# Performance work log

Hardware: AMD Instinct MI355X
Metric: run time of the kernel (lower is better)

Reference implementation:

```python
import jax, jax.numpy as jnp
import numpy as np

B, T, C, H = 4, 4096, 1024, 64

def setup_inputs() -> dict:
    key = jax.random.key(0)
    kx, kq, kk, kv = jax.random.split(key, 4)
    x = jax.random.normal(kx, (B, T, C), dtype=jnp.float32)
    Wq = jax.random.normal(kq, (C, H), dtype=jnp.float32) * (C ** -0.5)
    Wk = jax.random.normal(kk, (C, H), dtype=jnp.float32) * (C ** -0.5)
    Wv = jax.random.normal(kv, (C, H), dtype=jnp.float32) * (C ** -0.5)
    return {"x": x, "Wq": Wq, "Wk": Wk, "Wv": Wv}

def reference(x, Wq, Wk, Wv):
    # single-head causal attention, dropout p=0 (eval)
    q = jnp.einsum('btc,ch->bth', x, Wq)  # [B,T,H]
    k = jnp.einsum('btc,ch->bth', x, Wk)
    v = jnp.einsum('btc,ch->bth', x, Wv)
    scale = k.shape[-1] ** -0.5
    scores = jnp.einsum('bth,bsh->bts', q, k) * scale  # [B,T,T]
    causal = jnp.tril(jnp.ones((q.shape[1], q.shape[1]), dtype=bool))
    scores = jnp.where(causal, scores, -jnp.inf)
    weights = jax.nn.softmax(scores, axis=-1)
    out = jnp.einsum('bts,bsh->bth', weights, v)  # [B,T,H]
    return out
```

## Files before the change

kernel.cpp:

```cpp
#include <hip/hip_runtime.h>


typedef short  s16x8 __attribute__((ext_vector_type(8)));
typedef float  f32x4 __attribute__((ext_vector_type(4)));
typedef unsigned u32x2 __attribute__((ext_vector_type(2)));

constexpr int B = 4, T = 4096, C = 1024, H = 64;
constexpr int M = B * T;
constexpr float LOG2E = 1.44269504088896340736f;
constexpr float QSCALE = 0.125f * LOG2E;
constexpr float MBASE  = 4.0f * LOG2E;

__device__ __forceinline__ unsigned short f2bf(float f) {
    union { float f; unsigned u; } v; v.f = f;
    unsigned r = v.u + 0x7fffu + ((v.u >> 16) & 1u);
    return (unsigned short)(r >> 16);
}

__device__ __forceinline__ unsigned cvt_pk_bf16(float lo, float hi) {
    unsigned r;
    asm("v_cvt_pk_bf16_f32 %0, %1, %2" : "=v"(r) : "v"(lo), "v"(hi));
    return r;
}

__device__ __forceinline__ float vexp2(float x) {
    float r;
    asm("v_exp_f32 %0, %1" : "=v"(r) : "v"(x));
    return r;
}

__device__ __forceinline__ void gl_lds16(const void* g, void* l) {
    __builtin_amdgcn_global_load_lds(
        (const __attribute__((address_space(1))) unsigned*)g,
        (__attribute__((address_space(3))) unsigned*)l, 16, 0, 0);
}

__global__ void prep_w(const float* __restrict__ Wq, const float* __restrict__ Wk,
                       const float* __restrict__ Wv, unsigned short* __restrict__ Wt) {
    const int n = blockIdx.x;
    const float* W = (n < 64) ? Wq : (n < 128 ? Wk : Wv);
    const int col = n & 63;
    for (int k = threadIdx.x; k < C; k += blockDim.x)
        Wt[(size_t)n * C + k] = f2bf(W[(size_t)k * H + col]);
}

__global__ __launch_bounds__(512) void qkv_proj(
    const float* __restrict__ x, const unsigned short* __restrict__ Wt,
    unsigned short* __restrict__ Q, unsigned short* __restrict__ K,
    unsigned short* __restrict__ VT) {
    __shared__ __align__(16) unsigned short ldsA[2][32 * 64];
    __shared__ __align__(16) unsigned short ldsB[2][192 * 64];

    const int t = threadIdx.x, lane = t & 63, w = t >> 6;
    const int i = lane & 15, g = lane >> 4;
    const int rowbase = blockIdx.x * 32;
    const int rw = w & 1, nw = w >> 1;

    const int arow = t >> 3, aslot = t & 7;
    const float* aga = x + (size_t)(rowbase + arow) * C + ((aslot ^ (arow & 7)) * 8);
    const int awoff = arow * 64 + aslot * 8;
    const bool astage = (t < 256);

    const int brow8 = lane >> 3, bslot = lane & 7;
    const unsigned short* bga[3];
    int bn0[3];
#pragma unroll
    for (int j = 0; j < 3; ++j) {
        bn0[j] = w * 24 + j * 8;
        bga[j] = Wt + (size_t)(bn0[j] + brow8) * C + ((bslot ^ brow8) * 8);
    }

    f32x4 acc[3];
#pragma unroll
    for (int n = 0; n < 3; ++n) acc[n] = (f32x4){0.f, 0.f, 0.f, 0.f};

    {
#pragma unroll
        for (int j = 0; j < 3; ++j)
            gl_lds16(bga[j], &ldsB[0][bn0[j] * 64]);
        if (astage) {
            f32x4 a0 = *(const f32x4*)(aga);
            f32x4 a1 = *(const f32x4*)(aga + 4);
            union { unsigned u[4]; s16x8 v; } av;
            av.u[0] = cvt_pk_bf16(a0[0], a0[1]);
            av.u[1] = cvt_pk_bf16(a0[2], a0[3]);
            av.u[2] = cvt_pk_bf16(a1[0], a1[1]);
            av.u[3] = cvt_pk_bf16(a1[2], a1[3]);
            *(s16x8*)&ldsA[0][awoff] = av.v;
        }
    }
    __syncthreads();

    for (int it = 0; it < 16; ++it) {
        const int cur = it & 1, nxt = cur ^ 1;
        const int kc = (it + 1) * 64;
        f32x4 a0, a1;
        const bool more = (it < 15);
        if (more) {
            if (astage) {
                a0 = *(const f32x4*)(aga + kc);
                a1 = *(const f32x4*)(aga + kc + 4);
            }
#pragma unroll
            for (int j = 0; j < 3; ++j)
                gl_lds16(bga[j] + kc, &ldsB[nxt][bn0[j] * 64]);
        }
#pragma unroll
        for (int kst = 0; kst < 2; ++kst) {
            const int c = kst * 4 + g;
            s16x8 a = *(const s16x8*)&ldsA[cur][(rw * 16 + i) * 64 + ((c ^ (i & 7)) * 8)];
#pragma unroll
            for (int nt = 0; nt < 3; ++nt) {
                int n = nw * 48 + nt * 16 + i;
                s16x8 b = *(const s16x8*)&ldsB[cur][n * 64 + ((c ^ (i & 7)) * 8)];
                acc[nt] = __builtin_amdgcn_mfma_f32_16x16x32_bf16(a, b, acc[nt], 0, 0, 0);
            }
        }
        if (more && astage) {
            union { unsigned u[4]; s16x8 v; } av;
            av.u[0] = cvt_pk_bf16(a0[0], a0[1]);
            av.u[1] = cvt_pk_bf16(a0[2], a0[3]);
            av.u[2] = cvt_pk_bf16(a1[0], a1[1]);
            av.u[3] = cvt_pk_bf16(a1[2], a1[3]);
            *(s16x8*)&ldsA[nxt][awoff] = av.v;
        }
        __syncthreads();
    }

#pragma unroll
    for (int nt = 0; nt < 3; ++nt) {
        const int base = nw * 48 + nt * 16;
        const int n = base + i;
        if (base >= 128) {
            const int h = n - 128;
            const int bb = rowbase >> 12, tb = rowbase & 4095;
            u32x2 pk;
            pk[0] = cvt_pk_bf16(acc[nt][0], acc[nt][1]);
            pk[1] = cvt_pk_bf16(acc[nt][2], acc[nt][3]);
            *(u32x2*)(VT + (size_t)(bb * H + h) * T + tb + g * 8 + rw * 4) = pk;
        } else if (base >= 64) {
#pragma unroll
            for (int r = 0; r < 4; ++r)
                K[(size_t)(rowbase + rw * 16 + g * 4 + r) * H + (n - 64)] = f2bf(acc[nt][r]);
        } else {
#pragma unroll
            for (int r = 0; r < 4; ++r)
                Q[(size_t)(rowbase + rw * 16 + g * 4 + r) * H + n] = f2bf(acc[nt][r] * QSCALE);
        }
    }
}

template<int CUR>
__device__ __forceinline__ void attn_tile(
    int n, int nTiles, int sp, int q0w, int i, int g, int g4, int w,
    int r8, int sl, int sx,
    const unsigned short* Kb, const unsigned short* Vb,
    unsigned short (&ks)[3][64 * 64], unsigned short (&vs)[3][64 * 64],
    const s16x8& bqa0, const s16x8& bqa1, const s16x8& bqb0, const s16x8& bqb1,
    const s16x8& ones, const f32x4& minit,
    f32x4 (&oa)[4], f32x4 (&ob)[4], f32x4& al, f32x4& bl) {
    constexpr int NXT = (CUR + 2) % 3;
    const int kv = (sp + n * 8) * 64;
    const bool issue = (n + 2 < nTiles);

    if (issue) {
        const int kvn = kv + 1024;
#pragma unroll
        for (int j = 0; j < 2; ++j) {
            const int row = (w + j * 4) * 8 + r8;
            gl_lds16(Kb + (size_t)(kvn + row) * H + sx * 8, &ks[NXT][row * 64 + sl * 8]);
            gl_lds16(Vb + (size_t)row * T + kvn + sx * 8,   &vs[NXT][row * 64 + sl * 8]);
        }
    }

    if (kv <= q0w + 31) {
        s16x8 kb[8];
#pragma unroll
        for (int kst = 0; kst < 2; ++kst)
#pragma unroll
            for (int nt = 0; nt < 4; ++nt)
                kb[kst * 4 + nt] = *(const s16x8*)
                    &ks[CUR][(nt * 16 + i) * 64 + (((kst * 4 + g) ^ (i & 7)) * 8)];

        unsigned pa[8], pb2[8];

        {
            f32x4 s[4];
#pragma unroll
            for (int nt = 0; nt < 4; ++nt) {
                s[nt] = __builtin_amdgcn_mfma_f32_16x16x32_bf16(kb[nt], bqa0, minit, 0, 0, 0);
                s[nt] = __builtin_amdgcn_mfma_f32_16x16x32_bf16(kb[4 + nt], bqa1, s[nt], 0, 0, 0);
            }
            if (kv + 63 > q0w) {
                const int thr = q0w + i - kv;
#pragma unroll
                for (int nt = 0; nt < 4; ++nt)
#pragma unroll
                    for (int r = 0; r < 4; ++r)
                        if (nt * 16 + g4 + r > thr) s[nt][r] = -INFINITY;
            }
#pragma unroll
            for (int nt = 0; nt < 4; ++nt)
#pragma unroll
                for (int r = 0; r < 4; ++r)
                    s[nt][r] = vexp2(s[nt][r]);
#pragma unroll
            for (int nt = 0; nt < 4; ++nt) {
                pa[nt * 2]     = cvt_pk_bf16(s[nt][0], s[nt][1]);
                pa[nt * 2 + 1] = cvt_pk_bf16(s[nt][2], s[nt][3]);
            }
        }

        {
            f32x4 s[4];
#pragma unroll
            for (int nt = 0; nt < 4; ++nt) {
                s[nt] = __builtin_amdgcn_mfma_f32_16x16x32_bf16(kb[nt], bqb0, minit, 0, 0, 0);
                s[nt] = __builtin_amdgcn_mfma_f32_16x16x32_bf16(kb[4 + nt], bqb1, s[nt], 0, 0, 0);
            }
            if (kv + 63 > q0w + 16) {
                const int thr = q0w + 16 + i - kv;
#pragma unroll
                for (int nt = 0; nt < 4; ++nt)
#pragma unroll
                    for (int r = 0; r < 4; ++r)
                        if (nt * 16 + g4 + r > thr) s[nt][r] = -INFINITY;
            }
#pragma unroll
            for (int nt = 0; nt < 4; ++nt)
#pragma unroll
                for (int r = 0; r < 4; ++r)
                    s[nt][r] = vexp2(s[nt][r]);
#pragma unroll
            for (int nt = 0; nt < 4; ++nt) {
                pb2[nt * 2]     = cvt_pk_bf16(s[nt][0], s[nt][1]);
                pb2[nt * 2 + 1] = cvt_pk_bf16(s[nt][2], s[nt][3]);
            }
        }

        s16x8 vb[8];
#pragma unroll
        for (int kst = 0; kst < 2; ++kst)
#pragma unroll
            for (int nt = 0; nt < 4; ++nt)
                vb[kst * 4 + nt] = *(const s16x8*)
                    &vs[CUR][(nt * 16 + i) * 64 + (((kst * 4 + g) ^ (i & 7)) * 8)];

#pragma unroll
        for (int kst = 0; kst < 2; ++kst) {
            union { unsigned u[4]; s16x8 v; } fa, fb;
            fa.u[0] = pa[4 * kst];      fa.u[1] = pa[4 * kst + 1];
            fa.u[2] = pa[4 * kst + 2];  fa.u[3] = pa[4 * kst + 3];
            fb.u[0] = pb2[4 * kst];     fb.u[1] = pb2[4 * kst + 1];
            fb.u[2] = pb2[4 * kst + 2]; fb.u[3] = pb2[4 * kst + 3];
#pragma unroll
            for (int nt = 0; nt < 4; ++nt) {
                oa[nt] = __builtin_amdgcn_mfma_f32_16x16x32_bf16(vb[kst * 4 + nt], fa.v, oa[nt], 0, 0, 0);
                ob[nt] = __builtin_amdgcn_mfma_f32_16x16x32_bf16(vb[kst * 4 + nt], fb.v, ob[nt], 0, 0, 0);
            }
            al = __builtin_amdgcn_mfma_f32_16x16x32_bf16(ones, fa.v, al, 0, 0, 0);
            bl = __builtin_amdgcn_mfma_f32_16x16x32_bf16(ones, fb.v, bl, 0, 0, 0);
        }
    }

    if (issue) asm volatile("s_waitcnt vmcnt(4)\n\ts_barrier" ::: "memory");
    else       asm volatile("s_waitcnt vmcnt(0)\n\ts_barrier" ::: "memory");
}

__global__ __launch_bounds__(256) void attn(
    const unsigned short* __restrict__ Qg, const unsigned short* __restrict__ Kg,
    const unsigned short* __restrict__ VTg,
    unsigned short* __restrict__ Opb, float* __restrict__ lpart) {
    __shared__ __align__(16) unsigned short ks[3][64 * 64];
    __shared__ __align__(16) unsigned short vs[3][64 * 64];

    const int t = threadIdx.x, lane = t & 63, w = t >> 6;
    const int bid = blockIdx.x;
    const int b = bid & 3;
    const int sp = (bid >> 2) & 7;
    const int qt = 31 - (bid >> 5);
    const int q0 = qt * 128;
    const int q0w = q0 + w * 32;
    const int i = lane & 15, g = lane >> 4, g4 = g * 4;
    const int nkv = 2 * qt + 2;
    const int nTiles = (sp < nkv) ? ((nkv - sp + 7) >> 3) : 0;

    const unsigned short* Kb = Kg  + (size_t)b * T * H;
    const unsigned short* Vb = VTg + (size_t)b * H * T;

    const int r8 = lane >> 3, sl = lane & 7, sx = sl ^ r8;

    const unsigned short* QrowA = Qg + (size_t)(b * T + q0w + i) * H;
    s16x8 bqa0 = *(const s16x8*)(QrowA + g * 8);
    s16x8 bqa1 = *(const s16x8*)(QrowA + 32 + g * 8);
    const unsigned short* QrowB = QrowA + 16 * H;
    s16x8 bqb0 = *(const s16x8*)(QrowB + g * 8);
    s16x8 bqb1 = *(const s16x8*)(QrowB + 32 + g * 8);

    const f32x4 minit = (f32x4){-MBASE, -MBASE, -MBASE, -MBASE};
    s16x8 ones;
#pragma unroll
    for (int j = 0; j < 8; ++j) ones[j] = (short)0x3F80;

    f32x4 oa[4], ob[4];
#pragma unroll
    for (int nt = 0; nt < 4; ++nt) {
        oa[nt] = (f32x4){0.f, 0.f, 0.f, 0.f};
        ob[nt] = (f32x4){0.f, 0.f, 0.f, 0.f};
    }
    f32x4 al = (f32x4){0.f, 0.f, 0.f, 0.f};
    f32x4 bl = (f32x4){0.f, 0.f, 0.f, 0.f};

    if (nTiles > 0) {
        const int kv0 = sp * 64;
#pragma unroll
        for (int j = 0; j < 2; ++j) {
            const int row = (w + j * 4) * 8 + r8;
            gl_lds16(Kb + (size_t)(kv0 + row) * H + sx * 8, &ks[0][row * 64 + sl * 8]);
            gl_lds16(Vb + (size_t)row * T + kv0 + sx * 8,   &vs[0][row * 64 + sl * 8]);
        }
    }
    if (nTiles > 1) {
        const int kv1 = (sp + 8) * 64;
#pragma unroll
        for (int j = 0; j < 2; ++j) {
            const int row = (w + j * 4) * 8 + r8;
            gl_lds16(Kb + (size_t)(kv1 + row) * H + sx * 8, &ks[1][row * 64 + sl * 8]);
            gl_lds16(Vb + (size_t)row * T + kv1 + sx * 8,   &vs[1][row * 64 + sl * 8]);
        }
        asm volatile("s_waitcnt vmcnt(4)\n\ts_barrier" ::: "memory");
    } else {
        asm volatile("s_waitcnt vmcnt(0)\n\ts_barrier" ::: "memory");
    }

    {
        int n = 0;
        while (n < nTiles) {
            attn_tile<0>(n, nTiles, sp, q0w, i, g, g4, w, r8, sl, sx, Kb, Vb,
                         ks, vs, bqa0, bqa1, bqb0, bqb1, ones, minit, oa, ob, al, bl);
            if (++n >= nTiles) break;
            attn_tile<1>(n, nTiles, sp, q0w, i, g, g4, w, r8, sl, sx, Kb, Vb,
                         ks, vs, bqa0, bqa1, bqb0, bqb1, ones, minit, oa, ob, al, bl);
            if (++n >= nTiles) break;
            attn_tile<2>(n, nTiles, sp, q0w, i, g, g4, w, r8, sl, sx, Kb, Vb,
                         ks, vs, bqa0, bqa1, bqb0, bqb1, ones, minit, oa, ob, al, bl);
            ++n;
        }
    }

    unsigned short* opA = Opb + ((size_t)bid * 128 + w * 32 + i) * 64;
    unsigned short* opB = opA + 16 * 64;
#pragma unroll
    for (int nt = 0; nt < 4; ++nt) {
        u32x2 pk;
        pk[0] = cvt_pk_bf16(oa[nt][0], oa[nt][1]);
        pk[1] = cvt_pk_bf16(oa[nt][2], oa[nt][3]);
        *(u32x2*)(opA + nt * 16 + g4) = pk;
        pk[0] = cvt_pk_bf16(ob[nt][0], ob[nt][1]);
        pk[1] = cvt_pk_bf16(ob[nt][2], ob[nt][3]);
        *(u32x2*)(opB + nt * 16 + g4) = pk;
    }
    if (g == 0) {
        lpart[(size_t)bid * 128 + w * 32 + i]      = al[0];
        lpart[(size_t)bid * 128 + w * 32 + 16 + i] = bl[0];
    }
}

__global__ __launch_bounds__(256) void merge8(
    const unsigned short* __restrict__ Opb, const float* __restrict__ lpart,
    float* __restrict__ out) {
    const int idx = blockIdx.x * 256 + threadIdx.x;
    const int row = idx >> 4, c4 = (idx & 15) * 4;
    const int b = row >> 12, q = row & 4095;
    const int qt = q >> 7, r = q & 127;
    const int qti = 31 - qt;

    float L = 0.f;
    f32x4 o = (f32x4){0.f, 0.f, 0.f, 0.f};
#pragma unroll
    for (int sp = 0; sp < 8; ++sp) {
        const int bidp = qti * 32 + sp * 4 + b;
        L += lpart[(size_t)bidp * 128 + r];
        union { unsigned long long d; unsigned short s[4]; } v;
        v.d = *(const unsigned long long*)&Opb[((size_t)bidp * 128 + r) * 64 + c4];
#pragma unroll
        for (int k = 0; k < 4; ++k) {
            union { unsigned u; float f; } cv;
            cv.u = (unsigned)v.s[k] << 16;
            o[k] += cv.f;
        }
    }
    const float inv = 1.0f / L;
    f32x4 res = (f32x4){o[0] * inv, o[1] * inv, o[2] * inv, o[3] * inv};
    *(f32x4*)&out[(size_t)row * 64 + c4] = res;
}

extern "C" void kernel_launch(void* const* d_in, const int* in_sizes, int n_in,
                              void* d_out, int out_size, void* d_ws, size_t ws_size,
                              hipStream_t stream) {
    (void)in_sizes; (void)n_in; (void)out_size; (void)ws_size;
    const float* x  = (const float*)d_in[0];
    const float* Wq = (const float*)d_in[1];
    const float* Wk = (const float*)d_in[2];
    const float* Wv = (const float*)d_in[3];
    float* out = (float*)d_out;

    char* ws = (char*)d_ws;
    unsigned short* Q  = (unsigned short*)(ws);
    unsigned short* K  = (unsigned short*)(ws + (size_t)1 * M * H * 2);
    unsigned short* VT = (unsigned short*)(ws + (size_t)3 * M * H * 2);
    unsigned short* Wt = (unsigned short*)(ws + (size_t)4 * M * H * 2);
    unsigned short* Opb = (unsigned short*)(ws + (size_t)4 * M * H * 2 + 512 * 1024);
    float* lpart = (float*)(ws + (size_t)4 * M * H * 2 + 512 * 1024
                            + (size_t)1024 * 128 * 64 * 2);

    prep_w<<<192, 256, 0, stream>>>(Wq, Wk, Wv, Wt);
    qkv_proj<<<M / 32, 512, 0, stream>>>(x, Wt, Q, K, VT);
    attn<<<1024, 256, 0, stream>>>(Q, K, VT, Opb, lpart);
    merge8<<<1024, 256, 0, stream>>>(Opb, lpart, out);
}
```

Baseline: 50.27 us.

## Double attention query tile to 256 rows with 512-thread blocks

Each attention block now covers 256 query rows using 8 waves instead of 128 rows with 4 waves, so every K/V tile staged in LDS serves twice as many queries. Each thread now issues one K and one V async load per tile instead of two, and the wait counts are adjusted to match. Merge indexing and the workspace layout are updated for the new block shape. This halves global K/V traffic per query, at the cost of half as many blocks (512), larger and coarser causal work units, and possible load imbalance or lower occupancy.

```diff
diff --git a/kernel.cpp b/kernel.cpp
--- a/kernel.cpp
+++ b/kernel.cpp
@@ -152,8 +152,8 @@
 
 template<int CUR>
 __device__ __forceinline__ void attn_tile(
-    int n, int nTiles, int sp, int q0w, int i, int g, int g4, int w,
-    int r8, int sl, int sx,
+    int n, int nTiles, int sp, int q0w, int i, int g, int g4,
+    int srow, int sl, int sx,
     const unsigned short* Kb, const unsigned short* Vb,
     unsigned short (&ks)[3][64 * 64], unsigned short (&vs)[3][64 * 64],
     const s16x8& bqa0, const s16x8& bqa1, const s16x8& bqb0, const s16x8& bqb1,
@@ -165,12 +165,8 @@
 
     if (issue) {
         const int kvn = kv + 1024;
-#pragma unroll
-        for (int j = 0; j < 2; ++j) {
-            const int row = (w + j * 4) * 8 + r8;
-            gl_lds16(Kb + (size_t)(kvn + row) * H + sx * 8, &ks[NXT][row * 64 + sl * 8]);
-            gl_lds16(Vb + (size_t)row * T + kvn + sx * 8,   &vs[NXT][row * 64 + sl * 8]);
-        }
+        gl_lds16(Kb + (size_t)(kvn + srow) * H + sx * 8, &ks[NXT][srow * 64 + sl * 8]);
+        gl_lds16(Vb + (size_t)srow * T + kvn + sx * 8,   &vs[NXT][srow * 64 + sl * 8]);
     }
 
     if (kv <= q0w + 31) {
@@ -263,11 +259,11 @@
         }
     }
 
-    if (issue) asm volatile("s_waitcnt vmcnt(4)\n\ts_barrier" ::: "memory");
+    if (issue) asm volatile("s_waitcnt vmcnt(2)\n\ts_barrier" ::: "memory");
     else       asm volatile("s_waitcnt vmcnt(0)\n\ts_barrier" ::: "memory");
 }
 
-__global__ __launch_bounds__(256) void attn(
+__global__ __launch_bounds__(512) void attn(
     const unsigned short* __restrict__ Qg, const unsigned short* __restrict__ Kg,
     const unsigned short* __restrict__ VTg,
     unsigned short* __restrict__ Opb, float* __restrict__ lpart) {
@@ -278,17 +274,17 @@
     const int bid = blockIdx.x;
     const int b = bid & 3;
     const int sp = (bid >> 2) & 7;
-    const int qt = 31 - (bid >> 5);
-    const int q0 = qt * 128;
+    const int qt = 15 - (bid >> 5);
+    const int q0 = qt * 256;
     const int q0w = q0 + w * 32;
     const int i = lane & 15, g = lane >> 4, g4 = g * 4;
-    const int nkv = 2 * qt + 2;
+    const int nkv = 4 * qt + 4;
     const int nTiles = (sp < nkv) ? ((nkv - sp + 7) >> 3) : 0;
 
     const unsigned short* Kb = Kg  + (size_t)b * T * H;
     const unsigned short* Vb = VTg + (size_t)b * H * T;
 
-    const int r8 = lane >> 3, sl = lane & 7, sx = sl ^ r8;
+    const int srow = t >> 3, sl = t & 7, sx = sl ^ (srow & 7);
 
     const unsigned short* QrowA = Qg + (size_t)(b * T + q0w + i) * H;
     s16x8 bqa0 = *(const s16x8*)(QrowA + g * 8);
@@ -313,22 +309,14 @@
 
     if (nTiles > 0) {
         const int kv0 = sp * 64;
-#pragma unroll
-        for (int j = 0; j < 2; ++j) {
-            const int row = (w + j * 4) * 8 + r8;
-            gl_lds16(Kb + (size_t)(kv0 + row) * H + sx * 8, &ks[0][row * 64 + sl * 8]);
-            gl_lds16(Vb + (size_t)row * T + kv0 + sx * 8,   &vs[0][row * 64 + sl * 8]);
-        }
+        gl_lds16(Kb + (size_t)(kv0 + srow) * H + sx * 8, &ks[0][srow * 64 + sl * 8]);
+        gl_lds16(Vb + (size_t)srow * T + kv0 + sx * 8,   &vs[0][srow * 64 + sl * 8]);
     }
     if (nTiles > 1) {
         const int kv1 = (sp + 8) * 64;
-#pragma unroll
-        for (int j = 0; j < 2; ++j) {
-            const int row = (w + j * 4) * 8 + r8;
-            gl_lds16(Kb + (size_t)(kv1 + row) * H + sx * 8, &ks[1][row * 64 + sl * 8]);
-            gl_lds16(Vb + (size_t)row * T + kv1 + sx * 8,   &vs[1][row * 64 + sl * 8]);
-        }
-        asm volatile("s_waitcnt vmcnt(4)\n\ts_barrier" ::: "memory");
+        gl_lds16(Kb + (size_t)(kv1 + srow) * H + sx * 8, &ks[1][srow * 64 + sl * 8]);
+        gl_lds16(Vb + (size_t)srow * T + kv1 + sx * 8,   &vs[1][srow * 64 + sl * 8]);
+        asm volatile("s_waitcnt vmcnt(2)\n\ts_barrier" ::: "memory");
     } else {
         asm volatile("s_waitcnt vmcnt(0)\n\ts_barrier" ::: "memory");
     }
@@ -336,19 +324,19 @@
     {
         int n = 0;
         while (n < nTiles) {
-            attn_tile<0>(n, nTiles, sp, q0w, i, g, g4, w, r8, sl, sx, Kb, Vb,
+            attn_tile<0>(n, nTiles, sp, q0w, i, g, g4, srow, sl, sx, Kb, Vb,
                          ks, vs, bqa0, bqa1, bqb0, bqb1, ones, minit, oa, ob, al, bl);
             if (++n >= nTiles) break;
-            attn_tile<1>(n, nTiles, sp, q0w, i, g, g4, w, r8, sl, sx, Kb, Vb,
+            attn_tile<1>(n, nTiles, sp, q0w, i, g, g4, srow, sl, sx, Kb, Vb,
                          ks, vs, bqa0, bqa1, bqb0, bqb1, ones, minit, oa, ob, al, bl);
             if (++n >= nTiles) break;
-            attn_tile<2>(n, nTiles, sp, q0w, i, g, g4, w, r8, sl, sx, Kb, Vb,
+            attn_tile<2>(n, nTiles, sp, q0w, i, g, g4, srow, sl, sx, Kb, Vb,
                          ks, vs, bqa0, bqa1, bqb0, bqb1, ones, minit, oa, ob, al, bl);
             ++n;
         }
     }
 
-    unsigned short* opA = Opb + ((size_t)bid * 128 + w * 32 + i) * 64;
+    unsigned short* opA = Opb + ((size_t)bid * 256 + w * 32 + i) * 64;
     unsigned short* opB = opA + 16 * 64;
 #pragma unroll
     for (int nt = 0; nt < 4; ++nt) {
@@ -361,8 +349,8 @@
         *(u32x2*)(opB + nt * 16 + g4) = pk;
     }
     if (g == 0) {
-        lpart[(size_t)bid * 128 + w * 32 + i]      = al[0];
-        lpart[(size_t)bid * 128 + w * 32 + 16 + i] = bl[0];
+        lpart[(size_t)bid * 256 + w * 32 + i]      = al[0];
+        lpart[(size_t)bid * 256 + w * 32 + 16 + i] = bl[0];
     }
 }
 
@@ -372,17 +360,17 @@
     const int idx = blockIdx.x * 256 + threadIdx.x;
     const int row = idx >> 4, c4 = (idx & 15) * 4;
     const int b = row >> 12, q = row & 4095;
-    const int qt = q >> 7, r = q & 127;
-    const int qti = 31 - qt;
+    const int qt = q >> 8, r = q & 255;
+    const int qti = 15 - qt;
 
     float L = 0.f;
     f32x4 o = (f32x4){0.f, 0.f, 0.f, 0.f};
 #pragma unroll
     for (int sp = 0; sp < 8; ++sp) {
         const int bidp = qti * 32 + sp * 4 + b;
-        L += lpart[(size_t)bidp * 128 + r];
+        L += lpart[(size_t)bidp * 256 + r];
         union { unsigned long long d; unsigned short s[4]; } v;
-        v.d = *(const unsigned long long*)&Opb[((size_t)bidp * 128 + r) * 64 + c4];
+        v.d = *(const unsigned long long*)&Opb[((size_t)bidp * 256 + r) * 64 + c4];
 #pragma unroll
         for (int k = 0; k < 4; ++k) {
             union { unsigned u; float f; } cv;
@@ -412,10 +400,10 @@
     unsigned short* Wt = (unsigned short*)(ws + (size_t)4 * M * H * 2);
     unsigned short* Opb = (unsigned short*)(ws + (size_t)4 * M * H * 2 + 512 * 1024);
     float* lpart = (float*)(ws + (size_t)4 * M * H * 2 + 512 * 1024
-                            + (size_t)1024 * 128 * 64 * 2);
+                            + (size_t)512 * 256 * 64 * 2);
 
     prep_w<<<192, 256, 0, stream>>>(Wq, Wk, Wv, Wt);
     qkv_proj<<<M / 32, 512, 0, stream>>>(x, Wt, Q, K, VT);
-    attn<<<1024, 256, 0, stream>>>(Q, K, VT, Opb, lpart);
+    attn<<<512, 512, 0, stream>>>(Q, K, VT, Opb, lpart);
     merge8<<<1024, 256, 0, stream>>>(Opb, lpart, out);
 }
```

Measured after the change: 48.90 us (median of 2 runs). 1.03x faster.
